# Performance work log

Measured on AMD Instinct MI355X. Metric: run time of the kernel, lower is better.

## Reference

```python
import jax, jax.numpy as jnp
import numpy as np

B, N, I, H, NT = 512, 21, 256, 1024, 5  # batch, nodes, input, hidden, node types
EPS = 1e-12


def setup_inputs() -> dict:
    key = jax.random.key(0)
    ks = jax.random.split(key, 8)
    stdv = 1.0 / np.sqrt(H)
    return {
        "input": jax.random.normal(ks[0], (B, N, I), jnp.float32),
        "hx": 0.1 * jax.random.normal(ks[1], (B, N, H), jnp.float32),
        "cx": 0.1 * jax.random.normal(ks[2], (B, N, H), jnp.float32),
        "G": jnp.eye(N, dtype=jnp.float32) + 0.01 * jax.random.normal(ks[3], (N, N), jnp.float32),
        "weight_ih": jax.random.uniform(ks[4], (NT, 4 * H, I), jnp.float32, -stdv, stdv),
        "weight_hh": jax.random.uniform(ks[5], (NT, 4 * H, H), jnp.float32, -stdv, stdv),
        "bias_hh": jax.random.uniform(ks[6], (NT, 4 * H), jnp.float32, -stdv, stdv),
        "node_types": jax.random.randint(ks[7], (N,), 0, NT),
        "t": 3,
    }


def _l1_normalize_rows(g):
    # torch.nn.functional.normalize(g, p=1, dim=1)
    return g / jnp.maximum(jnp.sum(jnp.abs(g), axis=1, keepdims=True), EPS)


def _clockwork_phase(hidden_size, dtype):
    p = jnp.arange(hidden_size, dtype=dtype)
    p = p / p[-1] * 8.0 + 1.0
    return jnp.floor(p)  # values in {1..9}


def reference(input, hx, cx, G, weight_ih, weight_hh, bias_hh, node_types, t):
    # learn_influence=True -> gx = L1-row-normalized G
    gx = _l1_normalize_rows(G)

    # per-node-type weight gather: [N, 4H, I], [N, 4H, H], [N, 4H]
    w_ih = weight_ih[node_types]
    w_hh = weight_hh[node_types]
    b_hh = bias_hh[node_types]

    # gmm: einsum('ndo,bnd->bno', w.transpose(-2,-1), x) == einsum('noi,bni->bno', w, x)
    gates = (jnp.einsum('noi,bni->bno', w_ih, input)
             + jnp.einsum('noh,bnh->bno', w_hh, hx)
             + b_hh)
    # graph influence: matmul(gx, gates) over node dim -> [B, N, 4H]
    gates = jnp.einsum('mn,bno->bmo', gx, gates)

    ingate, forgetgate, cellgate, outgate = jnp.split(gates, 4, axis=2)
    ingate = jax.nn.sigmoid(ingate)
    forgetgate = jax.nn.sigmoid(forgetgate)
    cellgate = jnp.tanh(cellgate)
    outgate = jax.nn.sigmoid(outgate)

    phase = _clockwork_phase(hx.shape[-1], cx.dtype)
    c_mask = (jnp.remainder(jnp.float32(t) + 1.0, phase) < 0.01).astype(cx.dtype)

    cy = c_mask * (forgetgate * cx + ingate * cellgate) + (1.0 - c_mask) * cx
    hy = outgate * jnp.tanh(cy)

    # gx = gx + G_add (=0), then re-normalized because learn_influence=True
    gx_out = _l1_normalize_rows(gx)
    return hy, cy, gx_out
```

## Files before the change

### kernel.cpp

```cpp
#include <hip/hip_runtime.h>
#include <hip/hip_bf16.h>
#include <stdint.h>


typedef __bf16 bf16_t;
typedef __bf16 bf16x8 __attribute__((ext_vector_type(8)));
typedef float f32x4 __attribute__((ext_vector_type(4)));

#define NB 512
#define NN 21
#define NI 256
#define NH 1024
#define KDIM 1280
#define ODIM 4096
#define BNH (512ull * 21 * 1024)

__device__ inline void gld16(const void* g, const void* l) {
  __builtin_amdgcn_global_load_lds(
      (const __attribute__((address_space(1))) unsigned int*)g,
      (__attribute__((address_space(3))) unsigned int*)l, 16, 0, 0);
}

__device__ inline float sigmoid_fast(float x) {
  return 1.0f / (1.0f + __expf(-x));
}
__device__ inline float tanh_fast(float x) {
  float ax = fabsf(x);
  float e = __expf(2.0f * ax);
  float t = 1.0f - 2.0f / (e + 1.0f);
  return copysignf(t, x);
}

__global__ void gx_kernel(const float* __restrict__ G, float* __restrict__ gxw,
                          float* __restrict__ gxout) {
  int m = threadIdx.x;
  if (m < NN) {
    float s = 0.f;
    for (int j = 0; j < NN; j++) s += fabsf(G[m * NN + j]);
    s = fmaxf(s, 1e-12f);
    float row[NN];
    float s2 = 0.f;
    for (int j = 0; j < NN; j++) {
      row[j] = G[m * NN + j] / s;
      s2 += fabsf(row[j]);
    }
    s2 = fmaxf(s2, 1e-12f);
    for (int j = 0; j < NN; j++) {
      gxw[m * NN + j] = row[j];
      gxout[m * NN + j] = row[j] / s2;
    }
  }
}

__global__ __launch_bounds__(256) void pack_w(const float* __restrict__ wih,
                                              const float* __restrict__ whh,
                                              bf16_t* __restrict__ Wc) {
  int c = blockIdx.x * 256 + threadIdx.x;
  int k8 = c % (KDIM / 8);
  int row = c / (KDIM / 8);
  int k = k8 * 8;
  const float* src = (k < NI) ? (wih + (size_t)row * NI + k)
                              : (whh + (size_t)row * NH + (k - NI));
  float4 a = *(const float4*)src;
  float4 b = *(const float4*)(src + 4);
  bf16x8 o;
  o[0] = (bf16_t)a.x; o[1] = (bf16_t)a.y; o[2] = (bf16_t)a.z; o[3] = (bf16_t)a.w;
  o[4] = (bf16_t)b.x; o[5] = (bf16_t)b.y; o[6] = (bf16_t)b.z; o[7] = (bf16_t)b.w;
  *(bf16x8*)&Wc[(size_t)c * 8] = o;
}

__global__ __launch_bounds__(256) void pack_x(const float* __restrict__ input,
                                              const float* __restrict__ hx,
                                              bf16_t* __restrict__ Xc) {
  int c = blockIdx.x * 256 + threadIdx.x;
  int k8 = c % (KDIM / 8);
  int rest = c / (KDIM / 8);
  int n = rest / NB;
  int b = rest % NB;
  int k = k8 * 8;
  const float* src = (k < NI) ? (input + ((size_t)b * NN + n) * NI + k)
                              : (hx + ((size_t)b * NN + n) * NH + (k - NI));
  float4 a = *(const float4*)src;
  float4 d = *(const float4*)(src + 4);
  bf16x8 o;
  o[0] = (bf16_t)a.x; o[1] = (bf16_t)a.y; o[2] = (bf16_t)a.z; o[3] = (bf16_t)a.w;
  o[4] = (bf16_t)d.x; o[5] = (bf16_t)d.y; o[6] = (bf16_t)d.z; o[7] = (bf16_t)d.w;
  *(bf16x8*)&Xc[(size_t)c * 8] = o;
}

__global__ __launch_bounds__(256) void gemm_bt(const bf16_t* __restrict__ Xc,
                                               const bf16_t* __restrict__ Wc,
                                               const float* __restrict__ bhh,
                                               const int* __restrict__ node_types,
                                               bf16_t* __restrict__ gates) {
  __shared__ bf16_t As[128 * 32];
  __shared__ bf16_t Bs[128 * 32];

  const int n = blockIdx.z;
  const int tau = node_types[n];
  const bf16_t* A = Xc + (size_t)n * NB * KDIM;
  const bf16_t* B = Wc + (size_t)tau * ODIM * KDIM;

  const int tid = threadIdx.x;
  const int m0 = blockIdx.y * 128;
  const int n0 = blockIdx.x * 128;

  const int lane = tid & 63;
  const int wv = tid >> 6;
  const int wm = (wv >> 1) * 64;
  const int wn = (wv & 1) * 64;
  const int r = lane & 15;
  const int quad = lane >> 4;

  f32x4 acc[4][4];
#pragma unroll
  for (int i = 0; i < 4; i++)
#pragma unroll
    for (int j = 0; j < 4; j++) acc[i][j] = {0.f, 0.f, 0.f, 0.f};

  const int srow = tid >> 2;
  const int schunk = (tid & 3) * 8;

  for (int k0 = 0; k0 < KDIM; k0 += 32) {
    gld16(A + (size_t)(m0 + srow) * KDIM + k0 + schunk, (char*)As + tid * 16);
    gld16(A + (size_t)(m0 + 64 + srow) * KDIM + k0 + schunk, (char*)As + 4096 + tid * 16);
    gld16(B + (size_t)(n0 + srow) * KDIM + k0 + schunk, (char*)Bs + tid * 16);
    gld16(B + (size_t)(n0 + 64 + srow) * KDIM + k0 + schunk, (char*)Bs + 4096 + tid * 16);
    __syncthreads();

    bf16x8 af[4], bfr[4];
#pragma unroll
    for (int i = 0; i < 4; i++)
      af[i] = *(const bf16x8*)&As[(wm + i * 16 + r) * 32 + quad * 8];
#pragma unroll
    for (int j = 0; j < 4; j++)
      bfr[j] = *(const bf16x8*)&Bs[(wn + j * 16 + r) * 32 + quad * 8];
#pragma unroll
    for (int i = 0; i < 4; i++)
#pragma unroll
      for (int j = 0; j < 4; j++)
        acc[i][j] = __builtin_amdgcn_mfma_f32_16x16x32_bf16(af[i], bfr[j], acc[i][j], 0, 0, 0);
    __syncthreads();
  }

  float bv[4];
#pragma unroll
  for (int j = 0; j < 4; j++) bv[j] = bhh[tau * ODIM + n0 + wn + j * 16 + r];
#pragma unroll
  for (int i = 0; i < 4; i++) {
    int brow = m0 + wm + i * 16 + quad * 4;
#pragma unroll
    for (int j = 0; j < 4; j++) {
      int o = n0 + wn + j * 16 + r;
#pragma unroll
      for (int reg = 0; reg < 4; reg++) {
        int b = brow + reg;
        gates[((size_t)b * NN + n) * ODIM + o] = (bf16_t)(acc[i][j][reg] + bv[j]);
      }
    }
  }
}

__global__ __launch_bounds__(256) void mix_lin(bf16_t* __restrict__ gates,
                                               const float* __restrict__ gx) {
  __shared__ float gxs[NN * NN];
  __shared__ bf16_t gs[NN * 512];
  const int tid = threadIdx.x;
  for (int i = tid; i < NN * NN; i += 256) gxs[i] = gx[i];
  const int b = blockIdx.y;
  const int o0 = blockIdx.x * 512;
  const size_t base = (size_t)b * NN * ODIM + o0;

  for (int i = tid; i < NN * 64; i += 256) {
    int n = i / 64, c = i % 64;
    *(bf16x8*)&gs[n * 512 + c * 8] = *(const bf16x8*)&gates[base + (size_t)n * ODIM + c * 8];
  }
  __syncthreads();

  for (int i = tid; i < NN * 64; i += 256) {
    int m = i / 64, c = i % 64;
    float acc[8];
#pragma unroll
    for (int j = 0; j < 8; j++) acc[j] = 0.f;
    for (int n = 0; n < NN; n++) {
      float w = gxs[m * NN + n];
      bf16x8 v = *(const bf16x8*)&gs[n * 512 + c * 8];
#pragma unroll
      for (int j = 0; j < 8; j++) acc[j] += w * (float)v[j];
    }
    bf16x8 o;
#pragma unroll
    for (int j = 0; j < 8; j++) o[j] = (bf16_t)acc[j];
    *(bf16x8*)&gates[base + (size_t)m * ODIM + c * 8] = o;
  }
}

__global__ __launch_bounds__(256) void lstm_pw(const bf16_t* __restrict__ gates,
                                               const float* __restrict__ cx,
                                               const int* __restrict__ t_ptr,
                                               float* __restrict__ out) {
  int idx = blockIdx.x * 256 + threadIdx.x;
  int h8 = idx % 128;
  int bm = idx / 128;
  int h = h8 * 8;
  int t = t_ptr[0];
  size_t gbase = (size_t)bm * ODIM;
  bf16x8 vi = *(const bf16x8*)&gates[gbase + 0 * NH + h];
  bf16x8 vf = *(const bf16x8*)&gates[gbase + 1 * NH + h];
  bf16x8 vc = *(const bf16x8*)&gates[gbase + 2 * NH + h];
  bf16x8 vo = *(const bf16x8*)&gates[gbase + 3 * NH + h];
  size_t off = (size_t)bm * NH + h;
  float4 c0 = *(const float4*)&cx[off];
  float4 c1 = *(const float4*)&cx[off + 4];
  float cxv[8] = {c0.x, c0.y, c0.z, c0.w, c1.x, c1.y, c1.z, c1.w};
  float hy[8], cy[8];
  float tf = (float)(t + 1);
#pragma unroll
  for (int j = 0; j < 8; j++) {
    float phase = floorf(((float)(h + j)) / 1023.0f * 8.0f + 1.0f);
    bool cmask = fmodf(tf, phase) < 0.01f;
    float ig = sigmoid_fast((float)vi[j]);
    float fg = sigmoid_fast((float)vf[j]);
    float cg = tanh_fast((float)vc[j]);
    float og = sigmoid_fast((float)vo[j]);
    float c = cmask ? (fg * cxv[j] + ig * cg) : cxv[j];
    cy[j] = c;
    hy[j] = og * tanh_fast(c);
  }
  *(float4*)&out[off] = make_float4(hy[0], hy[1], hy[2], hy[3]);
  *(float4*)&out[off + 4] = make_float4(hy[4], hy[5], hy[6], hy[7]);
  *(float4*)&out[BNH + off] = make_float4(cy[0], cy[1], cy[2], cy[3]);
  *(float4*)&out[BNH + off + 4] = make_float4(cy[4], cy[5], cy[6], cy[7]);
}

extern "C" void kernel_launch(void* const* d_in, const int* in_sizes, int n_in,
                              void* d_out, int out_size, void* d_ws, size_t ws_size,
                              hipStream_t stream) {
  const float* input = (const float*)d_in[0];
  const float* hx = (const float*)d_in[1];
  const float* cx = (const float*)d_in[2];
  const float* G = (const float*)d_in[3];
  const float* wih = (const float*)d_in[4];
  const float* whh = (const float*)d_in[5];
  const float* bhh = (const float*)d_in[6];
  const int* node_types = (const int*)d_in[7];
  const int* t = (const int*)d_in[8];
  float* out = (float*)d_out;

  char* ws = (char*)d_ws;
  bf16_t* Wc = (bf16_t*)ws;
  bf16_t* Xc = (bf16_t*)(ws + 52428800);
  bf16_t* gates = (bf16_t*)(ws + 79953920);
  float* gxw = (float*)(ws + 168034304);

  gx_kernel<<<1, 64, 0, stream>>>(G, gxw, out + 2 * BNH);
  pack_w<<<(5 * ODIM * KDIM / 8) / 256, 256, 0, stream>>>(wih, whh, Wc);
  pack_x<<<(NN * NB * KDIM / 8) / 256, 256, 0, stream>>>(input, hx, Xc);
  dim3 gg(ODIM / 128, NB / 128, NN);
  gemm_bt<<<gg, 256, 0, stream>>>(Xc, Wc, bhh, node_types, gates);
  dim3 gm(ODIM / 512, NB);
  mix_lin<<<gm, 256, 0, stream>>>(gates, gxw);
  lstm_pw<<<(NB * NN * (NH / 8)) / 256, 256, 0, stream>>>(gates, cx, t, out);
}
```

Before: 458.8 us.

## Skip gate tiles masked by clockwork phase and fuse mixing with LSTM

Reads t on the device to decide which 128-wide hidden blocks have an active clockwork mask. For inactive blocks it skips packing the weights, the GEMM tiles and the mixing of the input, forget and cell gates. Only the output gate is computed for those blocks. The graph-mixing and LSTM pointwise kernels are merged into one kernel, so the mixed gates are never written back to global memory and re-read. This relies on the phase-to-block mapping lining up with 128-wide tiles, including the special case of the last element with phase 9.

```diff
diff --git a/kernel.cpp b/kernel.cpp
--- a/kernel.cpp
+++ b/kernel.cpp
@@ -29,6 +29,10 @@
   float e = __expf(2.0f * ax);
   float t = 1.0f - 2.0f / (e + 1.0f);
   return copysignf(t, x);
+}
+
+__device__ inline bool tile_needed(int g, int hb, int t1) {
+  return (g == 3) || (t1 % (hb + 1) == 0) || (hb == 7 && (t1 % 9) == 0);
 }
 
 __global__ void gx_kernel(const float* __restrict__ G, float* __restrict__ gxw,
@@ -54,19 +58,23 @@
 
 __global__ __launch_bounds__(256) void pack_w(const float* __restrict__ wih,
                                               const float* __restrict__ whh,
+                                              const int* __restrict__ t_ptr,
                                               bf16_t* __restrict__ Wc) {
   int c = blockIdx.x * 256 + threadIdx.x;
   int k8 = c % (KDIM / 8);
   int row = c / (KDIM / 8);
+  int o = row & (ODIM - 1);
+  int t1 = t_ptr[0] + 1;
+  if (!tile_needed((o >> 7) >> 3, (o >> 7) & 7, t1)) return;
   int k = k8 * 8;
   const float* src = (k < NI) ? (wih + (size_t)row * NI + k)
                               : (whh + (size_t)row * NH + (k - NI));
   float4 a = *(const float4*)src;
   float4 b = *(const float4*)(src + 4);
-  bf16x8 o;
-  o[0] = (bf16_t)a.x; o[1] = (bf16_t)a.y; o[2] = (bf16_t)a.z; o[3] = (bf16_t)a.w;
-  o[4] = (bf16_t)b.x; o[5] = (bf16_t)b.y; o[6] = (bf16_t)b.z; o[7] = (bf16_t)b.w;
-  *(bf16x8*)&Wc[(size_t)c * 8] = o;
+  bf16x8 v;
+  v[0] = (bf16_t)a.x; v[1] = (bf16_t)a.y; v[2] = (bf16_t)a.z; v[3] = (bf16_t)a.w;
+  v[4] = (bf16_t)b.x; v[5] = (bf16_t)b.y; v[6] = (bf16_t)b.z; v[7] = (bf16_t)b.w;
+  *(bf16x8*)&Wc[(size_t)c * 8] = v;
 }
 
 __global__ __launch_bounds__(256) void pack_x(const float* __restrict__ input,
@@ -82,17 +90,22 @@
                               : (hx + ((size_t)b * NN + n) * NH + (k - NI));
   float4 a = *(const float4*)src;
   float4 d = *(const float4*)(src + 4);
-  bf16x8 o;
-  o[0] = (bf16_t)a.x; o[1] = (bf16_t)a.y; o[2] = (bf16_t)a.z; o[3] = (bf16_t)a.w;
-  o[4] = (bf16_t)d.x; o[5] = (bf16_t)d.y; o[6] = (bf16_t)d.z; o[7] = (bf16_t)d.w;
-  *(bf16x8*)&Xc[(size_t)c * 8] = o;
+  bf16x8 v;
+  v[0] = (bf16_t)a.x; v[1] = (bf16_t)a.y; v[2] = (bf16_t)a.z; v[3] = (bf16_t)a.w;
+  v[4] = (bf16_t)d.x; v[5] = (bf16_t)d.y; v[6] = (bf16_t)d.z; v[7] = (bf16_t)d.w;
+  *(bf16x8*)&Xc[(size_t)c * 8] = v;
 }
 
 __global__ __launch_bounds__(256) void gemm_bt(const bf16_t* __restrict__ Xc,
                                                const bf16_t* __restrict__ Wc,
                                                const float* __restrict__ bhh,
                                                const int* __restrict__ node_types,
+                                               const int* __restrict__ t_ptr,
                                                bf16_t* __restrict__ gates) {
+  const int jt = blockIdx.x;
+  const int t1 = t_ptr[0] + 1;
+  if (!tile_needed(jt >> 3, jt & 7, t1)) return;
+
   __shared__ bf16_t As[128 * 32];
   __shared__ bf16_t Bs[128 * 32];
 
@@ -103,7 +116,7 @@
 
   const int tid = threadIdx.x;
   const int m0 = blockIdx.y * 128;
-  const int n0 = blockIdx.x * 128;
+  const int n0 = jt * 128;
 
   const int lane = tid & 63;
   const int wv = tid >> 6;
@@ -161,76 +174,86 @@
   }
 }
 
-__global__ __launch_bounds__(256) void mix_lin(bf16_t* __restrict__ gates,
-                                               const float* __restrict__ gx) {
+__global__ __launch_bounds__(256) void mix_lstm(const bf16_t* __restrict__ gates,
+                                                const float* __restrict__ gx,
+                                                const float* __restrict__ cx,
+                                                const int* __restrict__ t_ptr,
+                                                float* __restrict__ out) {
   __shared__ float gxs[NN * NN];
   __shared__ bf16_t gs[NN * 512];
   const int tid = threadIdx.x;
+  const int hb = blockIdx.x;
+  const int b = blockIdx.y;
+  const int t1 = t_ptr[0] + 1;
+  const bool need_ifc = (t1 % (hb + 1) == 0) || (hb == 7 && (t1 % 9) == 0);
+
   for (int i = tid; i < NN * NN; i += 256) gxs[i] = gx[i];
-  const int b = blockIdx.y;
-  const int o0 = blockIdx.x * 512;
-  const size_t base = (size_t)b * NN * ODIM + o0;
-
-  for (int i = tid; i < NN * 64; i += 256) {
-    int n = i / 64, c = i % 64;
-    *(bf16x8*)&gs[n * 512 + c * 8] = *(const bf16x8*)&gates[base + (size_t)n * ODIM + c * 8];
+
+  const int ng = need_ifc ? 4 : 1;
+  const int total = NN * 16 * ng;
+  for (int i = tid; i < total; i += 256) {
+    int n = i / (16 * ng);
+    int rr = i % (16 * ng);
+    int gi = rr / 16;
+    int h8 = rr % 16;
+    int g = need_ifc ? gi : 3;
+    *(bf16x8*)&gs[n * 512 + g * 128 + h8 * 8] =
+        *(const bf16x8*)&gates[((size_t)b * NN + n) * ODIM + g * NH + hb * 128 + h8 * 8];
   }
   __syncthreads();
 
-  for (int i = tid; i < NN * 64; i += 256) {
-    int m = i / 64, c = i % 64;
-    float acc[8];
-#pragma unroll
-    for (int j = 0; j < 8; j++) acc[j] = 0.f;
+  const float tf = (float)t1;
+  for (int i = tid; i < NN * 16; i += 256) {
+    int m = i >> 4;
+    int h8 = i & 15;
+    float so[8], si[8], sf[8], sc[8];
+#pragma unroll
+    for (int j = 0; j < 8; j++) { so[j] = 0.f; si[j] = 0.f; sf[j] = 0.f; sc[j] = 0.f; }
     for (int n = 0; n < NN; n++) {
       float w = gxs[m * NN + n];
-      bf16x8 v = *(const bf16x8*)&gs[n * 512 + c * 8];
-#pragma unroll
-      for (int j = 0; j < 8; j++) acc[j] += w * (float)v[j];
-    }
-    bf16x8 o;
-#pragma unroll
-    for (int j = 0; j < 8; j++) o[j] = (bf16_t)acc[j];
-    *(bf16x8*)&gates[base + (size_t)m * ODIM + c * 8] = o;
-  }
-}
-
-__global__ __launch_bounds__(256) void lstm_pw(const bf16_t* __restrict__ gates,
-                                               const float* __restrict__ cx,
-                                               const int* __restrict__ t_ptr,
-                                               float* __restrict__ out) {
-  int idx = blockIdx.x * 256 + threadIdx.x;
-  int h8 = idx % 128;
-  int bm = idx / 128;
-  int h = h8 * 8;
-  int t = t_ptr[0];
-  size_t gbase = (size_t)bm * ODIM;
-  bf16x8 vi = *(const bf16x8*)&gates[gbase + 0 * NH + h];
-  bf16x8 vf = *(const bf16x8*)&gates[gbase + 1 * NH + h];
-  bf16x8 vc = *(const bf16x8*)&gates[gbase + 2 * NH + h];
-  bf16x8 vo = *(const bf16x8*)&gates[gbase + 3 * NH + h];
-  size_t off = (size_t)bm * NH + h;
-  float4 c0 = *(const float4*)&cx[off];
-  float4 c1 = *(const float4*)&cx[off + 4];
-  float cxv[8] = {c0.x, c0.y, c0.z, c0.w, c1.x, c1.y, c1.z, c1.w};
-  float hy[8], cy[8];
-  float tf = (float)(t + 1);
-#pragma unroll
-  for (int j = 0; j < 8; j++) {
-    float phase = floorf(((float)(h + j)) / 1023.0f * 8.0f + 1.0f);
-    bool cmask = fmodf(tf, phase) < 0.01f;
-    float ig = sigmoid_fast((float)vi[j]);
-    float fg = sigmoid_fast((float)vf[j]);
-    float cg = tanh_fast((float)vc[j]);
-    float og = sigmoid_fast((float)vo[j]);
-    float c = cmask ? (fg * cxv[j] + ig * cg) : cxv[j];
-    cy[j] = c;
-    hy[j] = og * tanh_fast(c);
-  }
-  *(float4*)&out[off] = make_float4(hy[0], hy[1], hy[2], hy[3]);
-  *(float4*)&out[off + 4] = make_float4(hy[4], hy[5], hy[6], hy[7]);
-  *(float4*)&out[BNH + off] = make_float4(cy[0], cy[1], cy[2], cy[3]);
-  *(float4*)&out[BNH + off + 4] = make_float4(cy[4], cy[5], cy[6], cy[7]);
+      bf16x8 vo = *(const bf16x8*)&gs[n * 512 + 3 * 128 + h8 * 8];
+#pragma unroll
+      for (int j = 0; j < 8; j++) so[j] += w * (float)vo[j];
+      if (need_ifc) {
+        bf16x8 vi = *(const bf16x8*)&gs[n * 512 + 0 * 128 + h8 * 8];
+        bf16x8 vf = *(const bf16x8*)&gs[n * 512 + 1 * 128 + h8 * 8];
+        bf16x8 vc = *(const bf16x8*)&gs[n * 512 + 2 * 128 + h8 * 8];
+#pragma unroll
+        for (int j = 0; j < 8; j++) {
+          si[j] += w * (float)vi[j];
+          sf[j] += w * (float)vf[j];
+          sc[j] += w * (float)vc[j];
+        }
+      }
+    }
+    int h = hb * 128 + h8 * 8;
+    size_t off = ((size_t)b * NN + m) * NH + h;
+    float4 c0 = *(const float4*)&cx[off];
+    float4 c1 = *(const float4*)&cx[off + 4];
+    float cxv[8] = {c0.x, c0.y, c0.z, c0.w, c1.x, c1.y, c1.z, c1.w};
+    float hy[8], cy[8];
+#pragma unroll
+    for (int j = 0; j < 8; j++) {
+      float phase = floorf(((float)(h + j)) / 1023.0f * 8.0f + 1.0f);
+      bool cmask = fmodf(tf, phase) < 0.01f;
+      float og = sigmoid_fast(so[j]);
+      float c;
+      if (cmask) {
+        float ig = sigmoid_fast(si[j]);
+        float fg = sigmoid_fast(sf[j]);
+        float cg = tanh_fast(sc[j]);
+        c = fg * cxv[j] + ig * cg;
+      } else {
+        c = cxv[j];
+      }
+      cy[j] = c;
+      hy[j] = og * tanh_fast(c);
+    }
+    *(float4*)&out[off] = make_float4(hy[0], hy[1], hy[2], hy[3]);
+    *(float4*)&out[off + 4] = make_float4(hy[4], hy[5], hy[6], hy[7]);
+    *(float4*)&out[BNH + off] = make_float4(cy[0], cy[1], cy[2], cy[3]);
+    *(float4*)&out[BNH + off + 4] = make_float4(cy[4], cy[5], cy[6], cy[7]);
+  }
 }
 
 extern "C" void kernel_launch(void* const* d_in, const int* in_sizes, int n_in,
@@ -254,11 +277,10 @@
   float* gxw = (float*)(ws + 168034304);
 
   gx_kernel<<<1, 64, 0, stream>>>(G, gxw, out + 2 * BNH);
-  pack_w<<<(5 * ODIM * KDIM / 8) / 256, 256, 0, stream>>>(wih, whh, Wc);
+  pack_w<<<(5 * ODIM * KDIM / 8) / 256, 256, 0, stream>>>(wih, whh, t, Wc);
   pack_x<<<(NN * NB * KDIM / 8) / 256, 256, 0, stream>>>(input, hx, Xc);
   dim3 gg(ODIM / 128, NB / 128, NN);
-  gemm_bt<<<gg, 256, 0, stream>>>(Xc, Wc, bhh, node_types, gates);
-  dim3 gm(ODIM / 512, NB);
-  mix_lin<<<gm, 256, 0, stream>>>(gates, gxw);
-  lstm_pw<<<(NB * NN * (NH / 8)) / 256, 256, 0, stream>>>(gates, cx, t, out);
-}
+  gemm_bt<<<gg, 256, 0, stream>>>(Xc, Wc, bhh, node_types, t, gates);
+  dim3 gm(NH / 128, NB);
+  mix_lstm<<<gm, 256, 0, stream>>>(gates, gxw, cx, t, out);
+}
```

New measurement: 576.0 us. 25.5% more time.
